# Kernel tuning notes

Measured on AMD Instinct MI355X. Metric: run time of the kernel, lower is better.

The kernel has to match this reference:

```python
import math
import jax, jax.numpy as jnp
import numpy as np

NUM_HEADS = 8

def setup_inputs() -> dict:
    key = jax.random.key(0)
    ks = jax.random.split(key, 4)
    b, c, T, H, W = 8, 512, 8, 16, 16
    data_dim = T * H * W  # 2048
    x = jax.random.normal(ks[0], (b, c, T, H, W), dtype=jnp.float32)
    pos_emb = jax.random.normal(ks[1], (c, data_dim + 1), dtype=jnp.float32) / math.sqrt(c)
    w_qkv = jax.random.normal(ks[2], (3 * c, c), dtype=jnp.float32) * (1.0 / math.sqrt(c))
    b_qkv = jnp.zeros((3 * c,), dtype=jnp.float32)
    w_c = jax.random.normal(ks[3], (c, c), dtype=jnp.float32) * (1.0 / math.sqrt(c))
    b_c = jnp.zeros((c,), dtype=jnp.float32)
    return {"x": x, "pos_emb": pos_emb, "w_qkv": w_qkv, "b_qkv": b_qkv, "w_c": w_c, "b_c": b_c}

def reference(x, pos_emb, w_qkv, b_qkv, w_c, b_c):
    b, c = x.shape[0], x.shape[1]
    xf = x.reshape(b, c, -1)                                   # [b, c, THW]
    xf = jnp.concatenate([xf.mean(axis=-1, keepdims=True), xf], axis=-1)  # [b, c, T+1]
    xf = xf + pos_emb[None].astype(xf.dtype)
    qkv = jnp.einsum('oc,bct->bot', w_qkv, xf) + b_qkv[None, :, None]      # [b, 3c, L]
    L = qkv.shape[-1]
    ch = c // NUM_HEADS
    q, k, v = jnp.split(qkv, 3, axis=1)
    q = q.reshape(b * NUM_HEADS, ch, L)
    k = k.reshape(b * NUM_HEADS, ch, L)
    v = v.reshape(b * NUM_HEADS, ch, L)
    scale = 1.0 / math.sqrt(math.sqrt(ch))
    w = jnp.einsum('bct,bcs->bts', q * scale, k * scale)        # [bH, L, L]
    w = jax.nn.softmax(w.astype(jnp.float32), axis=-1).astype(qkv.dtype)
    a = jnp.einsum('bts,bcs->bct', w, v).reshape(b, c, L)       # [b, c, L]
    out = jnp.einsum('oc,bct->bot', w_c, a) + b_c[None, :, None]
    return out[:, :, 0]                                         # [b, out_dim]
```

## Files before the change

kernel.cpp:

```cpp
#include <hip/hip_runtime.h>

#define B 8
#define C 512
#define D 2048
#define L 2049
#define NH 8
#define CH 64
#define NLT 32
#define TLD 513

__device__ __forceinline__ float wave_sum(float v) {
  #pragma unroll
  for (int off = 32; off; off >>= 1) v += __shfl_down(v, off);
  return v;
}
__device__ __forceinline__ float wave_max(float v) {
  #pragma unroll
  for (int off = 32; off; off >>= 1) v = fmaxf(v, __shfl_down(v, off));
  return v;
}
__device__ __forceinline__ float lane_bcast(float v, int l) {
  return __uint_as_float(__builtin_amdgcn_readlane(__float_as_uint(v), l));
}

__global__ void __launch_bounds__(256) k_mean(const float* __restrict__ x,
                                              const float* __restrict__ pos,
                                              float* __restrict__ mps_g) {
  int row = blockIdx.x;
  const float4* xr = reinterpret_cast<const float4*>(x + (size_t)row * D);
  float s = 0.f;
  #pragma unroll
  for (int i = 0; i < 2; ++i) {
    float4 v = xr[threadIdx.x + i * 256];
    s += (v.x + v.y) + (v.z + v.w);
  }
  __shared__ float red[4];
  s = wave_sum(s);
  if ((threadIdx.x & 63) == 0) red[threadIdx.x >> 6] = s;
  __syncthreads();
  if (threadIdx.x == 0)
    mps_g[row] = (red[0] + red[1] + red[2] + red[3]) * (1.0f / D)
               + pos[(size_t)(row & (C - 1)) * L];
}

__global__ void __launch_bounds__(256) k_qu(const float* __restrict__ wqkv,
                                            const float* __restrict__ bqkv,
                                            const float* __restrict__ mps_g,
                                            float* __restrict__ u,
                                            float* __restrict__ logit0) {
  int bh = blockIdx.x, b = bh >> 3, h = bh & 7;
  int tid = threadIdx.x, wid = tid >> 6, lane = tid & 63;
  __shared__ float mps[C];
  __shared__ float q0s[CH];
  __shared__ float us[C];
  __shared__ float red[4];
  for (int c = tid; c < C; c += 256) mps[c] = mps_g[b * C + c];
  __syncthreads();
  for (int j = wid; j < CH; j += 4) {
    const float* wr = wqkv + (size_t)(h * CH + j) * C;
    float acc = 0.f;
    #pragma unroll
    for (int k = 0; k < 8; ++k) acc += wr[lane + k * 64] * mps[lane + k * 64];
    acc = wave_sum(acc);
    if (lane == 0) q0s[j] = acc + bqkv[h * CH + j];
  }
  __syncthreads();
  float a0 = 0.f, a1 = 0.f;
  #pragma unroll 4
  for (int j = 0; j < CH; ++j) {
    float qv = q0s[j];
    const float* wkr = wqkv + (size_t)(C + h * CH + j) * C;
    a0 += qv * wkr[tid];
    a1 += qv * wkr[tid + 256];
  }
  a0 *= 0.125f; a1 *= 0.125f;
  us[tid] = a0; us[tid + 256] = a1;
  u[(size_t)bh * C + tid] = a0;
  u[(size_t)bh * C + tid + 256] = a1;
  __syncthreads();
  float p = us[tid] * mps[tid] + us[tid + 256] * mps[tid + 256];
  p = wave_sum(p);
  if (lane == 0) red[wid] = p;
  __syncthreads();
  if (tid == 0) logit0[bh] = red[0] + red[1] + red[2] + red[3];
}

__global__ void __launch_bounds__(512, 2) k_fused_lx(
    const float* __restrict__ x, const float* __restrict__ pos,
    const float* __restrict__ u_g,
    float* __restrict__ xpart, float* __restrict__ mpart, float* __restrict__ spart) {
  __shared__ float tile[64][TLD];
  __shared__ float rlds[8][NH][64];
  __shared__ float e_t[64][9];
  int lt = blockIdx.x, b = blockIdx.y;
  int tid = threadIdx.x, wid = tid >> 6, lane = tid & 63;
  int cg = wid * 64;
  int col = lt * 64 + lane;

  float ureg[NH];
  #pragma unroll
  for (int h = 0; h < NH; ++h) ureg[h] = u_g[(size_t)(b * NH + h) * C + cg + lane];

  const float* xp = x + ((size_t)(b * C + cg)) * D + col;
  const float* pp = pos + (size_t)cg * L + col + 1;

  float v_arr[64];
  #pragma unroll
  for (int cc = 0; cc < 64; ++cc) v_arr[cc] = xp[(size_t)cc * D];
  #pragma unroll
  for (int cc = 0; cc < 64; ++cc) v_arr[cc] += pp[(size_t)cc * L];

  float acc[NH];
  #pragma unroll
  for (int h = 0; h < NH; ++h) acc[h] = 0.f;
  #pragma unroll
  for (int cc = 0; cc < 64; ++cc) {
    tile[lane][cg + cc] = v_arr[cc];
    #pragma unroll
    for (int h = 0; h < NH; ++h) acc[h] += lane_bcast(ureg[h], cc) * v_arr[cc];
  }
  #pragma unroll
  for (int h = 0; h < NH; ++h) rlds[wid][h][lane] = acc[h];
  __syncthreads();

  {
    int h = wid;
    float lg = 0.f;
    #pragma unroll
    for (int w = 0; w < 8; ++w) lg += rlds[w][h][lane];
    float m = wave_max(lg);
    m = lane_bcast(m, 0);
    float e = __expf(lg - m);
    float s = wave_sum(e);
    e_t[lane][h] = e;
    if (lane == 0) {
      mpart[(b * NH + h) * NLT + lt] = m;
      spart[(b * NH + h) * NLT + lt] = s;
    }
  }
  __syncthreads();

  float epre[NH];
  #pragma unroll
  for (int h = 0; h < NH; ++h) epre[h] = e_t[lane][h];
  float a2[NH];
  #pragma unroll
  for (int h = 0; h < NH; ++h) a2[h] = 0.f;
  #pragma unroll
  for (int half = 0; half < 2; ++half) {
    float xv[32];
    #pragma unroll
    for (int i = 0; i < 32; ++i) xv[i] = tile[half * 32 + i][tid];
    #pragma unroll
    for (int i = 0; i < 32; ++i) {
      #pragma unroll
      for (int h = 0; h < NH; ++h)
        a2[h] += lane_bcast(epre[h], half * 32 + i) * xv[i];
    }
  }
  #pragma unroll
  for (int h = 0; h < NH; ++h)
    xpart[(((size_t)b * NLT + lt) * NH + h) * C + tid] = a2[h];
}

__global__ void __launch_bounds__(512) k_a0(
    const float* __restrict__ xpart, const float* __restrict__ mpart,
    const float* __restrict__ spart, const float* __restrict__ logit0,
    const float* __restrict__ mps_g,
    const float* __restrict__ wqkv, const float* __restrict__ bqkv,
    float* __restrict__ a0v) {
  int bh = blockIdx.x, b = bh >> 3, h = bh & 7;
  int tid = threadIdx.x, wid = tid >> 6, lane = tid & 63;
  __shared__ float row[C];
  float lg0 = logit0[bh];
  float mt = (lane < NLT) ? mpart[bh * NLT + lane] : -3.0e38f;
  float M = fmaxf(lane_bcast(wave_max(mt), 0), lg0);
  float rr = (lane < NLT) ? __expf(mt - M) : 0.f;
  float st = (lane < NLT) ? spart[bh * NLT + lane] * rr : 0.f;
  float S = lane_bcast(wave_sum(st), 0) + __expf(lg0 - M);
  float Sinv = 1.0f / S;
  float acc = 0.f;
  #pragma unroll
  for (int t = 0; t < NLT; ++t)
    acc += xpart[(((size_t)b * NLT + t) * NH + h) * C + tid] * lane_bcast(rr, t);
  acc = (acc + __expf(lg0 - M) * mps_g[b * C + tid]) * Sinv;
  row[tid] = acc;
  __syncthreads();
  float xr[8];
  #pragma unroll
  for (int k = 0; k < 8; ++k) xr[k] = row[k * 64 + lane];
  #pragma unroll 2
  for (int j = 0; j < 8; ++j) {
    int o = h * CH + wid * 8 + j;
    const float* wr = wqkv + (size_t)(2 * C + o) * C;
    float d = 0.f;
    #pragma unroll
    for (int k = 0; k < 8; ++k) d += wr[k * 64 + lane] * xr[k];
    d = wave_sum(d);
    if (lane == 0) a0v[b * C + o] = d + bqkv[2 * C + o];
  }
}

__global__ void __launch_bounds__(512) k_out(const float* __restrict__ wc,
                                             const float* __restrict__ bc,
                                             const float* __restrict__ a0v,
                                             float* __restrict__ out) {
  int bid = blockIdx.x, b = bid >> 3, og = (bid & 7) * 64;
  int tid = threadIdx.x, wid = tid >> 6, lane = tid & 63;
  __shared__ float row[C];
  row[tid] = a0v[b * C + tid];
  __syncthreads();
  float ar[8];
  #pragma unroll
  for (int k = 0; k < 8; ++k) ar[k] = row[k * 64 + lane];
  #pragma unroll 2
  for (int j = 0; j < 8; ++j) {
    int o = og + wid * 8 + j;
    const float* wr = wc + (size_t)o * C;
    float d = 0.f;
    #pragma unroll
    for (int k = 0; k < 8; ++k) d += wr[k * 64 + lane] * ar[k];
    d = wave_sum(d);
    if (lane == 0) out[b * C + o] = d + bc[o];
  }
}

extern "C" void kernel_launch(void* const* d_in, const int* in_sizes, int n_in,
                              void* d_out, int out_size, void* d_ws, size_t ws_size,
                              hipStream_t stream) {
  const float* x    = (const float*)d_in[0];
  const float* pos  = (const float*)d_in[1];
  const float* wqkv = (const float*)d_in[2];
  const float* bqkv = (const float*)d_in[3];
  const float* wc   = (const float*)d_in[4];
  const float* bc   = (const float*)d_in[5];
  float* out = (float*)d_out;
  float* ws  = (float*)d_ws;

  float* mps_g  = ws;
  float* u      = ws + 4096;
  float* logit0 = ws + 36864;
  float* mpart  = ws + 36928;
  float* spart  = ws + 38976;
  float* a0v    = ws + 41024;
  float* xpart  = ws + 45120;

  hipLaunchKernelGGL(k_mean,     dim3(B * C),  dim3(256), 0, stream, x, pos, mps_g);
  hipLaunchKernelGGL(k_qu,       dim3(B * NH), dim3(256), 0, stream, wqkv, bqkv, mps_g, u, logit0);
  hipLaunchKernelGGL(k_fused_lx, dim3(NLT, B), dim3(512), 0, stream, x, pos, u, xpart, mpart, spart);
  hipLaunchKernelGGL(k_a0,       dim3(B * NH), dim3(512), 0, stream, xpart, mpart, spart, logit0,
                     mps_g, wqkv, bqkv, a0v);
  hipLaunchKernelGGL(k_out,      dim3(B * NH), dim3(512), 0, stream, wc, bc, a0v, out);
}
```

Before: 58.76 us.

## Load x tile directly into LDS via global_load_lds and transpose tile layout

The fused logits/accumulate kernel now streams x straight from global memory into LDS with the global_load_lds builtin, skipping the 64-register staging array. The tile is stored as [channel][column] with padding, pos is added in place in 16-row batches, and the second pass reads float2 pairs per channel row. The intent is to cut VGPR pressure and the LDS-write transpose cost. In exchange the tile grows and launch bounds drop to one block per CU, which may reduce occupancy, and the float2 reads along a row with stride 66 may cause bank conflicts.

```diff
diff --git a/kernel.cpp b/kernel.cpp
--- a/kernel.cpp
+++ b/kernel.cpp
@@ -7,7 +7,7 @@
 #define NH 8
 #define CH 64
 #define NLT 32
-#define TLD 513
+#define XPAD 66
 
 __device__ __forceinline__ float wave_sum(float v) {
   #pragma unroll
@@ -21,6 +21,11 @@
 }
 __device__ __forceinline__ float lane_bcast(float v, int l) {
   return __uint_as_float(__builtin_amdgcn_readlane(__float_as_uint(v), l));
+}
+__device__ __forceinline__ void glds4(const float* g, float* l) {
+  __builtin_amdgcn_global_load_lds(
+      (const __attribute__((address_space(1))) unsigned int*)g,
+      (__attribute__((address_space(3))) unsigned int*)l, 4, 0, 0);
 }
 
 __global__ void __launch_bounds__(256) k_mean(const float* __restrict__ x,
@@ -85,11 +90,11 @@
   if (tid == 0) logit0[bh] = red[0] + red[1] + red[2] + red[3];
 }
 
-__global__ void __launch_bounds__(512, 2) k_fused_lx(
+__global__ void __launch_bounds__(512, 1) k_fused_lx(
     const float* __restrict__ x, const float* __restrict__ pos,
     const float* __restrict__ u_g,
     float* __restrict__ xpart, float* __restrict__ mpart, float* __restrict__ spart) {
-  __shared__ float tile[64][TLD];
+  __shared__ float xt[C][XPAD];
   __shared__ float rlds[8][NH][64];
   __shared__ float e_t[64][9];
   int lt = blockIdx.x, b = blockIdx.y;
@@ -97,27 +102,36 @@
   int cg = wid * 64;
   int col = lt * 64 + lane;
 
+  const float* gp = x + ((size_t)(b * C + cg)) * D + col;
+  #pragma unroll
+  for (int cc = 0; cc < 64; ++cc)
+    glds4(gp + (size_t)cc * D, &xt[cg + cc][0]);
+
   float ureg[NH];
   #pragma unroll
   for (int h = 0; h < NH; ++h) ureg[h] = u_g[(size_t)(b * NH + h) * C + cg + lane];
 
-  const float* xp = x + ((size_t)(b * C + cg)) * D + col;
-  const float* pp = pos + (size_t)cg * L + col + 1;
-
-  float v_arr[64];
-  #pragma unroll
-  for (int cc = 0; cc < 64; ++cc) v_arr[cc] = xp[(size_t)cc * D];
-  #pragma unroll
-  for (int cc = 0; cc < 64; ++cc) v_arr[cc] += pp[(size_t)cc * L];
+  asm volatile("s_waitcnt vmcnt(0)" ::: "memory");
+  __builtin_amdgcn_sched_barrier(0);
 
   float acc[NH];
   #pragma unroll
   for (int h = 0; h < NH; ++h) acc[h] = 0.f;
-  #pragma unroll
-  for (int cc = 0; cc < 64; ++cc) {
-    tile[lane][cg + cc] = v_arr[cc];
-    #pragma unroll
-    for (int h = 0; h < NH; ++h) acc[h] += lane_bcast(ureg[h], cc) * v_arr[cc];
+  const float* pb = pos + (size_t)cg * L + col + 1;
+  #pragma unroll
+  for (int g = 0; g < 4; ++g) {
+    float parr[16];
+    #pragma unroll
+    for (int i = 0; i < 16; ++i)
+      parr[i] = pb[(size_t)(g * 16 + i) * L];
+    #pragma unroll
+    for (int i = 0; i < 16; ++i) {
+      const int cc = g * 16 + i;
+      float xf = xt[cg + cc][lane] + parr[i];
+      xt[cg + cc][lane] = xf;
+      #pragma unroll
+      for (int h = 0; h < NH; ++h) acc[h] += lane_bcast(ureg[h], cc) * xf;
+    }
   }
   #pragma unroll
   for (int h = 0; h < NH; ++h) rlds[wid][h][lane] = acc[h];
@@ -148,14 +162,16 @@
   for (int h = 0; h < NH; ++h) a2[h] = 0.f;
   #pragma unroll
   for (int half = 0; half < 2; ++half) {
-    float xv[32];
-    #pragma unroll
-    for (int i = 0; i < 32; ++i) xv[i] = tile[half * 32 + i][tid];
-    #pragma unroll
-    for (int i = 0; i < 32; ++i) {
+    float2 xv[16];
+    #pragma unroll
+    for (int i = 0; i < 16; ++i)
+      xv[i] = *reinterpret_cast<const float2*>(&xt[tid][half * 32 + i * 2]);
+    #pragma unroll
+    for (int i = 0; i < 16; ++i) {
       #pragma unroll
       for (int h = 0; h < NH; ++h)
-        a2[h] += lane_bcast(epre[h], half * 32 + i) * xv[i];
+        a2[h] += lane_bcast(epre[h], half * 32 + 2 * i) * xv[i].x
+               + lane_bcast(epre[h], half * 32 + 2 * i + 1) * xv[i].y;
     }
   }
   #pragma unroll
```

After: 59.61 us. No clear change (+1.4%).

## Split fused logits/softmax-weighted-sum into separate logits and xbar kernels

Applied to the files above, without the earlier changes.

Replaces the single fused kernel, which did online-softmax partials per 64-column tile, with two kernels. The first computes logits split over channel quarters with float4 loads. The second does a full-row softmax in LDS and the exp-weighted sum over x. This removes the large transposed LDS tile, the per-tile max/sum merging in k_a0, and the heavy register pressure. The cost is reading x and pos twice from global memory, plus an extra launch and an extra partial-logit buffer round trip.

```diff
diff --git a/kernel.cpp b/kernel.cpp
--- a/kernel.cpp
+++ b/kernel.cpp
@@ -6,8 +6,7 @@
 #define L 2049
 #define NH 8
 #define CH 64
-#define NLT 32
-#define TLD 513
+#define NCQ 4
 
 __device__ __forceinline__ float wave_sum(float v) {
   #pragma unroll
@@ -85,106 +84,132 @@
   if (tid == 0) logit0[bh] = red[0] + red[1] + red[2] + red[3];
 }
 
-__global__ void __launch_bounds__(512, 2) k_fused_lx(
+__global__ void __launch_bounds__(512) k_logits(
     const float* __restrict__ x, const float* __restrict__ pos,
-    const float* __restrict__ u_g,
-    float* __restrict__ xpart, float* __restrict__ mpart, float* __restrict__ spart) {
-  __shared__ float tile[64][TLD];
-  __shared__ float rlds[8][NH][64];
-  __shared__ float e_t[64][9];
-  int lt = blockIdx.x, b = blockIdx.y;
-  int tid = threadIdx.x, wid = tid >> 6, lane = tid & 63;
-  int cg = wid * 64;
-  int col = lt * 64 + lane;
-
-  float ureg[NH];
-  #pragma unroll
-  for (int h = 0; h < NH; ++h) ureg[h] = u_g[(size_t)(b * NH + h) * C + cg + lane];
-
-  const float* xp = x + ((size_t)(b * C + cg)) * D + col;
-  const float* pp = pos + (size_t)cg * L + col + 1;
-
-  float v_arr[64];
-  #pragma unroll
-  for (int cc = 0; cc < 64; ++cc) v_arr[cc] = xp[(size_t)cc * D];
-  #pragma unroll
-  for (int cc = 0; cc < 64; ++cc) v_arr[cc] += pp[(size_t)cc * L];
-
-  float acc[NH];
-  #pragma unroll
-  for (int h = 0; h < NH; ++h) acc[h] = 0.f;
-  #pragma unroll
-  for (int cc = 0; cc < 64; ++cc) {
-    tile[lane][cg + cc] = v_arr[cc];
-    #pragma unroll
-    for (int h = 0; h < NH; ++h) acc[h] += lane_bcast(ureg[h], cc) * v_arr[cc];
-  }
-  #pragma unroll
-  for (int h = 0; h < NH; ++h) rlds[wid][h][lane] = acc[h];
-  __syncthreads();
-
+    const float* __restrict__ u_g, float* __restrict__ wpart) {
+  __shared__ float us[NH][128];
+  __shared__ float4 rlds[8][NH][64];
+  int lt = blockIdx.x, b = blockIdx.y, cq = blockIdx.z;
+  int tid = threadIdx.x, w = tid >> 6, lane = tid & 63;
+  for (int idx = tid; idx < NH * 128; idx += 512) {
+    int h = idx >> 7, cc = idx & 127;
+    us[h][cc] = u_g[(size_t)(b * NH + h) * C + cq * 128 + cc];
+  }
+  __syncthreads();
+  float4 acc[NH];
+  #pragma unroll
+  for (int h = 0; h < NH; ++h) acc[h] = make_float4(0.f, 0.f, 0.f, 0.f);
+  int c0 = cq * 128 + w * 16;
+  int jb = lt * 256 + lane * 4;
+  const float4* x4 = reinterpret_cast<const float4*>(x)
+                   + ((size_t)(b * C + c0)) * (D / 4) + (jb >> 2);
+  const float* pb = pos + (size_t)c0 * L + jb + 1;
+  #pragma unroll
+  for (int r = 0; r < 16; ++r) {
+    float4 v = x4[(size_t)r * (D / 4)];
+    const float* pr = pb + (size_t)r * L;
+    v.x += pr[0]; v.y += pr[1]; v.z += pr[2]; v.w += pr[3];
+    #pragma unroll
+    for (int h = 0; h < NH; ++h) {
+      float uu = us[h][w * 16 + r];
+      acc[h].x += uu * v.x; acc[h].y += uu * v.y;
+      acc[h].z += uu * v.z; acc[h].w += uu * v.w;
+    }
+  }
+  #pragma unroll
+  for (int h = 0; h < NH; ++h) rlds[w][h][lane] = acc[h];
+  __syncthreads();
+  int h = tid >> 6, slot = tid & 63;
+  float4 s = rlds[0][h][slot];
+  #pragma unroll
+  for (int w2 = 1; w2 < 8; ++w2) {
+    float4 t = rlds[w2][h][slot];
+    s.x += t.x; s.y += t.y; s.z += t.z; s.w += t.w;
+  }
+  reinterpret_cast<float4*>(
+      wpart + ((size_t)((b * NH + h) * NCQ + cq)) * (size_t)D + lt * 256)[slot] = s;
+}
+
+__global__ void __launch_bounds__(512) k_xbar(
+    const float* __restrict__ x, const float* __restrict__ pos,
+    const float* __restrict__ wpart, const float* __restrict__ logit0,
+    const float* __restrict__ mps_g, float* __restrict__ xbar) {
+  __shared__ float eL[NH][D];
+  __shared__ float sinv[NH], w0e[NH];
+  int cc = blockIdx.x, b = blockIdx.y;
+  int tid = threadIdx.x, w = tid >> 6, lane = tid & 63;
   {
-    int h = wid;
-    float lg = 0.f;
-    #pragma unroll
-    for (int w = 0; w < 8; ++w) lg += rlds[w][h][lane];
-    float m = wave_max(lg);
-    m = lane_bcast(m, 0);
-    float e = __expf(lg - m);
-    float s = wave_sum(e);
-    e_t[lane][h] = e;
-    if (lane == 0) {
-      mpart[(b * NH + h) * NLT + lt] = m;
-      spart[(b * NH + h) * NLT + lt] = s;
-    }
-  }
-  __syncthreads();
-
-  float epre[NH];
-  #pragma unroll
-  for (int h = 0; h < NH; ++h) epre[h] = e_t[lane][h];
-  float a2[NH];
-  #pragma unroll
-  for (int h = 0; h < NH; ++h) a2[h] = 0.f;
-  #pragma unroll
-  for (int half = 0; half < 2; ++half) {
-    float xv[32];
-    #pragma unroll
-    for (int i = 0; i < 32; ++i) xv[i] = tile[half * 32 + i][tid];
-    #pragma unroll
-    for (int i = 0; i < 32; ++i) {
+    int h = w, bh = b * NH + h;
+    const float* wp = wpart + (size_t)(bh * NCQ) * D;
+    float s_arr[32];
+    float m = -3.0e38f;
+    #pragma unroll
+    for (int k = 0; k < 32; ++k) {
+      int l = k * 64 + lane;
+      float s = wp[l] + wp[D + l] + wp[2 * D + l] + wp[3 * D + l];
+      s_arr[k] = s;
+      m = fmaxf(m, s);
+    }
+    float lg0 = logit0[bh];
+    float M = fmaxf(lane_bcast(wave_max(m), 0), lg0);
+    float ssum = 0.f;
+    #pragma unroll
+    for (int k = 0; k < 32; ++k) {
+      float e = __expf(s_arr[k] - M);
+      eL[h][k * 64 + lane] = e;
+      ssum += e;
+    }
+    float e0 = __expf(lg0 - M);
+    float S = lane_bcast(wave_sum(ssum), 0) + e0;
+    if (lane == 0) { sinv[h] = 1.0f / S; w0e[h] = e0; }
+  }
+  __syncthreads();
+  int c0 = cc * 16 + w * 2;
+  float accr[2][NH];
+  #pragma unroll
+  for (int r = 0; r < 2; ++r)
+    #pragma unroll
+    for (int h = 0; h < NH; ++h) accr[r][h] = 0.f;
+  const float4* x4 = reinterpret_cast<const float4*>(x) + ((size_t)(b * C + c0)) * (D / 4);
+  const float* pb = pos + (size_t)c0 * L + 1;
+  #pragma unroll
+  for (int k = 0; k < 8; ++k) {
+    int fi = k * 64 + lane;
+    float4 e4[NH];
+    #pragma unroll
+    for (int h = 0; h < NH; ++h)
+      e4[h] = reinterpret_cast<const float4*>(eL[h])[fi];
+    #pragma unroll
+    for (int r = 0; r < 2; ++r) {
+      float4 xv = x4[(size_t)r * (D / 4) + fi];
+      const float* pr = pb + (size_t)r * L + fi * 4;
+      xv.x += pr[0]; xv.y += pr[1]; xv.z += pr[2]; xv.w += pr[3];
       #pragma unroll
       for (int h = 0; h < NH; ++h)
-        a2[h] += lane_bcast(epre[h], half * 32 + i) * xv[i];
-    }
-  }
-  #pragma unroll
-  for (int h = 0; h < NH; ++h)
-    xpart[(((size_t)b * NLT + lt) * NH + h) * C + tid] = a2[h];
+        accr[r][h] += e4[h].x * xv.x + e4[h].y * xv.y
+                    + e4[h].z * xv.z + e4[h].w * xv.w;
+    }
+  }
+  #pragma unroll
+  for (int r = 0; r < 2; ++r) {
+    int c = c0 + r;
+    float mv = mps_g[b * C + c];
+    #pragma unroll
+    for (int h = 0; h < NH; ++h) {
+      float t = wave_sum(accr[r][h]);
+      if (lane == 0)
+        xbar[(size_t)(b * NH + h) * C + c] = (t + w0e[h] * mv) * sinv[h];
+    }
+  }
 }
 
 __global__ void __launch_bounds__(512) k_a0(
-    const float* __restrict__ xpart, const float* __restrict__ mpart,
-    const float* __restrict__ spart, const float* __restrict__ logit0,
-    const float* __restrict__ mps_g,
-    const float* __restrict__ wqkv, const float* __restrict__ bqkv,
-    float* __restrict__ a0v) {
+    const float* __restrict__ xbarg, const float* __restrict__ wqkv,
+    const float* __restrict__ bqkv, float* __restrict__ a0v) {
   int bh = blockIdx.x, b = bh >> 3, h = bh & 7;
   int tid = threadIdx.x, wid = tid >> 6, lane = tid & 63;
   __shared__ float row[C];
-  float lg0 = logit0[bh];
-  float mt = (lane < NLT) ? mpart[bh * NLT + lane] : -3.0e38f;
-  float M = fmaxf(lane_bcast(wave_max(mt), 0), lg0);
-  float rr = (lane < NLT) ? __expf(mt - M) : 0.f;
-  float st = (lane < NLT) ? spart[bh * NLT + lane] * rr : 0.f;
-  float S = lane_bcast(wave_sum(st), 0) + __expf(lg0 - M);
-  float Sinv = 1.0f / S;
-  float acc = 0.f;
-  #pragma unroll
-  for (int t = 0; t < NLT; ++t)
-    acc += xpart[(((size_t)b * NLT + t) * NH + h) * C + tid] * lane_bcast(rr, t);
-  acc = (acc + __expf(lg0 - M) * mps_g[b * C + tid]) * Sinv;
-  row[tid] = acc;
+  row[tid] = xbarg[(size_t)bh * C + tid];
   __syncthreads();
   float xr[8];
   #pragma unroll
@@ -240,15 +265,14 @@
   float* mps_g  = ws;
   float* u      = ws + 4096;
   float* logit0 = ws + 36864;
-  float* mpart  = ws + 36928;
-  float* spart  = ws + 38976;
-  float* a0v    = ws + 41024;
-  float* xpart  = ws + 45120;
-
-  hipLaunchKernelGGL(k_mean,     dim3(B * C),  dim3(256), 0, stream, x, pos, mps_g);
-  hipLaunchKernelGGL(k_qu,       dim3(B * NH), dim3(256), 0, stream, wqkv, bqkv, mps_g, u, logit0);
-  hipLaunchKernelGGL(k_fused_lx, dim3(NLT, B), dim3(512), 0, stream, x, pos, u, xpart, mpart, spart);
-  hipLaunchKernelGGL(k_a0,       dim3(B * NH), dim3(512), 0, stream, xpart, mpart, spart, logit0,
-                     mps_g, wqkv, bqkv, a0v);
-  hipLaunchKernelGGL(k_out,      dim3(B * NH), dim3(512), 0, stream, wc, bc, a0v, out);
-}
+  float* a0v    = ws + 36928;
+  float* xbarg  = ws + 41024;
+  float* wpart  = ws + 73792;
+
+  hipLaunchKernelGGL(k_mean,   dim3(B * C),       dim3(256), 0, stream, x, pos, mps_g);
+  hipLaunchKernelGGL(k_qu,     dim3(B * NH),      dim3(256), 0, stream, wqkv, bqkv, mps_g, u, logit0);
+  hipLaunchKernelGGL(k_logits, dim3(8, B, NCQ),   dim3(512), 0, stream, x, pos, u, wpart);
+  hipLaunchKernelGGL(k_xbar,   dim3(32, B),       dim3(512), 0, stream, x, pos, wpart, logit0, mps_g, xbarg);
+  hipLaunchKernelGGL(k_a0,     dim3(B * NH),      dim3(512), 0, stream, xbarg, wqkv, bqkv, a0v);
+  hipLaunchKernelGGL(k_out,    dim3(B * NH),      dim3(512), 0, stream, wc, bc, a0v, out);
+}
```

Result: slower. 85.80 us (+46.0%).

## Realign pos_emb into workspace and restructure fused logit kernel with float4 loads

Applied to the files above, without the earlier changes.

k_mean now also copies pos_emb (skipping column 0) into an aligned workspace buffer so the fused kernel can read both x and pos with float4 vector loads. The fused kernel drops the large transposed LDS tile and keeps each thread's 16 float4 values in registers. It computes head logits from u staged in shared memory and reduces the weighted sums for xpart with cross-lane shuffles instead of readlane broadcasts. This cuts LDS usage and uncoalesced scalar loads, at the cost of an extra 4 MB copy of pos each call and many shuffle reductions with lane-predicated scalar stores.

```diff
diff --git a/kernel.cpp b/kernel.cpp
--- a/kernel.cpp
+++ b/kernel.cpp
@@ -7,7 +7,6 @@
 #define NH 8
 #define CH 64
 #define NLT 32
-#define TLD 513
 
 __device__ __forceinline__ float wave_sum(float v) {
   #pragma unroll
@@ -25,8 +24,16 @@
 
 __global__ void __launch_bounds__(256) k_mean(const float* __restrict__ x,
                                               const float* __restrict__ pos,
-                                              float* __restrict__ mps_g) {
+                                              float* __restrict__ mps_g,
+                                              float* __restrict__ pos_sh) {
   int row = blockIdx.x;
+  if (row < C) {
+    const float* src = pos + (size_t)row * L + 1;
+    float* dst = pos_sh + (size_t)row * D;
+    #pragma unroll
+    for (int i = 0; i < 8; ++i)
+      dst[threadIdx.x + i * 256] = src[threadIdx.x + i * 256];
+  }
   const float4* xr = reinterpret_cast<const float4*>(x + (size_t)row * D);
   float s = 0.f;
   #pragma unroll
@@ -85,51 +92,64 @@
   if (tid == 0) logit0[bh] = red[0] + red[1] + red[2] + red[3];
 }
 
-__global__ void __launch_bounds__(512, 2) k_fused_lx(
-    const float* __restrict__ x, const float* __restrict__ pos,
+__global__ void __launch_bounds__(512, 2) k_fused(
+    const float* __restrict__ x, const float* __restrict__ pos_sh,
     const float* __restrict__ u_g,
     float* __restrict__ xpart, float* __restrict__ mpart, float* __restrict__ spart) {
-  __shared__ float tile[64][TLD];
+  __shared__ float us[NH][C];
   __shared__ float rlds[8][NH][64];
-  __shared__ float e_t[64][9];
+  __shared__ float e_t[64][NH + 1];
   int lt = blockIdx.x, b = blockIdx.y;
-  int tid = threadIdx.x, wid = tid >> 6, lane = tid & 63;
-  int cg = wid * 64;
-  int col = lt * 64 + lane;
-
-  float ureg[NH];
-  #pragma unroll
-  for (int h = 0; h < NH; ++h) ureg[h] = u_g[(size_t)(b * NH + h) * C + cg + lane];
-
-  const float* xp = x + ((size_t)(b * C + cg)) * D + col;
-  const float* pp = pos + (size_t)cg * L + col + 1;
-
-  float v_arr[64];
-  #pragma unroll
-  for (int cc = 0; cc < 64; ++cc) v_arr[cc] = xp[(size_t)cc * D];
-  #pragma unroll
-  for (int cc = 0; cc < 64; ++cc) v_arr[cc] += pp[(size_t)cc * L];
-
-  float acc[NH];
-  #pragma unroll
-  for (int h = 0; h < NH; ++h) acc[h] = 0.f;
-  #pragma unroll
-  for (int cc = 0; cc < 64; ++cc) {
-    tile[lane][cg + cc] = v_arr[cc];
-    #pragma unroll
-    for (int h = 0; h < NH; ++h) acc[h] += lane_bcast(ureg[h], cc) * v_arr[cc];
-  }
-  #pragma unroll
-  for (int h = 0; h < NH; ++h) rlds[wid][h][lane] = acc[h];
+  int tid = threadIdx.x, w = tid >> 6, lane = tid & 63;
+  int ls = lane & 15, cs = lane >> 4;
+  int cg = w * 64;
+
+  #pragma unroll
+  for (int h = 0; h < NH; ++h) us[h][tid] = u_g[(size_t)(b * NH + h) * C + tid];
+  __syncthreads();
+
+  const float4* x4 = reinterpret_cast<const float4*>(x);
+  const float4* p4 = reinterpret_cast<const float4*>(pos_sh);
+  const int fbase = lt * 16 + ls;
+
+  float4 v[16];
+  float4 acc[NH];
+  #pragma unroll
+  for (int h = 0; h < NH; ++h) acc[h] = make_float4(0.f, 0.f, 0.f, 0.f);
+  #pragma unroll
+  for (int k = 0; k < 16; ++k) {
+    int row = cg + 4 * k + cs;
+    float4 xv = x4[((size_t)(b * C) + row) * (D / 4) + fbase];
+    float4 pv = p4[(size_t)row * (D / 4) + fbase];
+    xv.x += pv.x; xv.y += pv.y; xv.z += pv.z; xv.w += pv.w;
+    v[k] = xv;
+    #pragma unroll
+    for (int h = 0; h < NH; ++h) {
+      float uu = us[h][row];
+      acc[h].x += uu * xv.x; acc[h].y += uu * xv.y;
+      acc[h].z += uu * xv.z; acc[h].w += uu * xv.w;
+    }
+  }
+  #pragma unroll
+  for (int h = 0; h < NH; ++h) {
+    acc[h].x += __shfl_xor(acc[h].x, 16); acc[h].y += __shfl_xor(acc[h].y, 16);
+    acc[h].z += __shfl_xor(acc[h].z, 16); acc[h].w += __shfl_xor(acc[h].w, 16);
+    acc[h].x += __shfl_xor(acc[h].x, 32); acc[h].y += __shfl_xor(acc[h].y, 32);
+    acc[h].z += __shfl_xor(acc[h].z, 32); acc[h].w += __shfl_xor(acc[h].w, 32);
+  }
+  if (cs == 0) {
+    #pragma unroll
+    for (int h = 0; h < NH; ++h)
+      *reinterpret_cast<float4*>(&rlds[w][h][ls * 4]) = acc[h];
+  }
   __syncthreads();
 
   {
-    int h = wid;
+    int h = w;
     float lg = 0.f;
     #pragma unroll
-    for (int w = 0; w < 8; ++w) lg += rlds[w][h][lane];
-    float m = wave_max(lg);
-    m = lane_bcast(m, 0);
+    for (int w2 = 0; w2 < 8; ++w2) lg += rlds[w2][h][lane];
+    float m = lane_bcast(wave_max(lg), 0);
     float e = __expf(lg - m);
     float s = wave_sum(e);
     e_t[lane][h] = e;
@@ -140,27 +160,21 @@
   }
   __syncthreads();
 
-  float epre[NH];
-  #pragma unroll
-  for (int h = 0; h < NH; ++h) epre[h] = e_t[lane][h];
-  float a2[NH];
-  #pragma unroll
-  for (int h = 0; h < NH; ++h) a2[h] = 0.f;
-  #pragma unroll
-  for (int half = 0; half < 2; ++half) {
-    float xv[32];
-    #pragma unroll
-    for (int i = 0; i < 32; ++i) xv[i] = tile[half * 32 + i][tid];
-    #pragma unroll
-    for (int i = 0; i < 32; ++i) {
-      #pragma unroll
-      for (int h = 0; h < NH; ++h)
-        a2[h] += lane_bcast(epre[h], half * 32 + i) * xv[i];
+  #pragma unroll
+  for (int h = 0; h < NH; ++h) {
+    float e0 = e_t[ls * 4 + 0][h], e1 = e_t[ls * 4 + 1][h];
+    float e2 = e_t[ls * 4 + 2][h], e3 = e_t[ls * 4 + 3][h];
+    #pragma unroll
+    for (int k = 0; k < 16; ++k) {
+      float s = e0 * v[k].x + e1 * v[k].y + e2 * v[k].z + e3 * v[k].w;
+      s += __shfl_xor(s, 1);
+      s += __shfl_xor(s, 2);
+      s += __shfl_xor(s, 4);
+      s += __shfl_xor(s, 8);
+      if (ls == 0)
+        xpart[(((size_t)b * NLT + lt) * NH + h) * C + cg + 4 * k + cs] = s;
     }
   }
-  #pragma unroll
-  for (int h = 0; h < NH; ++h)
-    xpart[(((size_t)b * NLT + lt) * NH + h) * C + tid] = a2[h];
 }
 
 __global__ void __launch_bounds__(512) k_a0(
@@ -180,7 +194,7 @@
   float S = lane_bcast(wave_sum(st), 0) + __expf(lg0 - M);
   float Sinv = 1.0f / S;
   float acc = 0.f;
-  #pragma unroll
+  #pragma unroll 8
   for (int t = 0; t < NLT; ++t)
     acc += xpart[(((size_t)b * NLT + t) * NH + h) * C + tid] * lane_bcast(rr, t);
   acc = (acc + __expf(lg0 - M) * mps_g[b * C + tid]) * Sinv;
@@ -243,12 +257,13 @@
   float* mpart  = ws + 36928;
   float* spart  = ws + 38976;
   float* a0v    = ws + 41024;
-  float* xpart  = ws + 45120;
-
-  hipLaunchKernelGGL(k_mean,     dim3(B * C),  dim3(256), 0, stream, x, pos, mps_g);
-  hipLaunchKernelGGL(k_qu,       dim3(B * NH), dim3(256), 0, stream, wqkv, bqkv, mps_g, u, logit0);
-  hipLaunchKernelGGL(k_fused_lx, dim3(NLT, B), dim3(512), 0, stream, x, pos, u, xpart, mpart, spart);
-  hipLaunchKernelGGL(k_a0,       dim3(B * NH), dim3(512), 0, stream, xpart, mpart, spart, logit0,
+  float* pos_sh = ws + 45120;
+  float* xpart  = ws + 1093696;
+
+  hipLaunchKernelGGL(k_mean,  dim3(B * C),  dim3(256), 0, stream, x, pos, mps_g, pos_sh);
+  hipLaunchKernelGGL(k_qu,    dim3(B * NH), dim3(256), 0, stream, wqkv, bqkv, mps_g, u, logit0);
+  hipLaunchKernelGGL(k_fused, dim3(NLT, B), dim3(512), 0, stream, x, pos_sh, u, xpart, mpart, spart);
+  hipLaunchKernelGGL(k_a0,    dim3(B * NH), dim3(512), 0, stream, xpart, mpart, spart, logit0,
                      mps_g, wqkv, bqkv, a0v);
-  hipLaunchKernelGGL(k_out,      dim3(B * NH), dim3(512), 0, stream, wc, bc, a0v, out);
-}
+  hipLaunchKernelGGL(k_out,   dim3(B * NH), dim3(512), 0, stream, wc, bc, a0v, out);
+}
```

Result: slower. 72.12 us (+22.7%).
